# Optimization experiments

Hardware: AMD Instinct MI355X
Metric: run time of the kernel (lower is better)

Reference implementation:

```python
import jax, jax.numpy as jnp
import numpy as np

OUT_H, OUT_W = 128, 128


def _meshgrid(h, w):
    # normalized grid in [-1, 1], homogeneous coords: [3, h*w]
    x_t = jnp.tile(jnp.linspace(-1.0, 1.0, w)[None, :], (h, 1))
    y_t = jnp.tile(jnp.linspace(-1.0, 1.0, h)[:, None], (1, w))
    ones = jnp.ones((h * w,), dtype=jnp.float32)
    return jnp.stack([x_t.ravel(), y_t.ravel(), ones], axis=0)


def _bilinear_sample(im, x, y):
    # im: [B, H, W, C]; x, y: [B, N] pixel-space coords (transformer.py convention)
    B, H, W, C = im.shape
    # map from [-1,1] to pixel coords: x = (x + 1) * W / 2 (original transformer.py)
    x = (x + 1.0) * (W / 2.0)
    y = (y + 1.0) * (H / 2.0)

    x0 = jnp.floor(x).astype(jnp.int32)
    x1 = x0 + 1
    y0 = jnp.floor(y).astype(jnp.int32)
    y1 = y0 + 1

    x0 = jnp.clip(x0, 0, W - 1)
    x1 = jnp.clip(x1, 0, W - 1)
    y0 = jnp.clip(y0, 0, H - 1)
    y1 = jnp.clip(y1, 0, H - 1)

    bidx = jnp.arange(B, dtype=jnp.int32)[:, None]  # [B, 1] broadcasts over N
    Ia = im[bidx, y0, x0]  # [B, N, C]
    Ib = im[bidx, y1, x0]
    Ic = im[bidx, y0, x1]
    Id = im[bidx, y1, x1]

    x0f = x0.astype(jnp.float32)
    x1f = x1.astype(jnp.float32)
    y0f = y0.astype(jnp.float32)
    y1f = y1.astype(jnp.float32)

    wa = ((x1f - x) * (y1f - y))[..., None]
    wb = ((x1f - x) * (y - y0f))[..., None]
    wc = ((x - x0f) * (y1f - y))[..., None]
    wd = ((x - x0f) * (y - y0f))[..., None]

    return wa * Ia + wb * Ib + wc * Ic + wd * Id  # [B, N, C]


def setup_inputs() -> dict:
    key = jax.random.key(0)
    k1, k2 = jax.random.split(key)
    B = 2048
    image = jax.random.uniform(k1, (B, 128, 128, 3), dtype=jnp.float32)
    # near-identity homographies so sampling grids stay numerically sane
    H = jnp.eye(3, dtype=jnp.float32)[None] + 0.1 * jax.random.normal(
        k2, (B, 3, 3), dtype=jnp.float32)
    return {"image": image, "H": H}


def reference(image, H):
    # SpatialTransformer.call: take channel 0, projective warp, bilinear sample
    im = image[:, :, :, 0:1]  # [B, 128, 128, 1]
    B = im.shape[0]
    grid = _meshgrid(OUT_H, OUT_W)  # [3, N]
    T = jnp.einsum('bij,jn->bin', H, grid)  # [B, 3, N]
    z = T[:, 2]
    xs = T[:, 0] / z
    ys = T[:, 1] / z
    out = _bilinear_sample(im, xs, ys)  # [B, N, 1]
    return out.reshape(-1, OUT_H, OUT_W, 1)
```

## Files before the change

kernel.cpp:

```cpp
#include <hip/hip_runtime.h>


#define IMG_H 128
#define IMG_W 128

typedef float f32x2 __attribute__((ext_vector_type(2)));

__global__ __launch_bounds__(256) void st_warp_kernel(
    const float* __restrict__ img,
    const float* __restrict__ Hm,
    float* __restrict__ out)
{
    const int b  = blockIdx.x >> 5;
    const int n0 = ((blockIdx.x & 31) << 9) | (threadIdx.x << 1);
    const int i  = n0 >> 7;
    const int j0 = n0 & 127;

    const float* Hb = Hm + b * 9;
    const float h00 = Hb[0], h01 = Hb[1], h02 = Hb[2];
    const float h10 = Hb[3], h11 = Hb[4], h12 = Hb[5];
    const float h20 = Hb[6], h21 = Hb[7], h22 = Hb[8];

    const float step = 2.0f / 127.0f;
    const float yt = -1.0f + step * (float)i;
    const float* imb = img + (size_t)b * (IMG_H * IMG_W * 3);

    const float xtA = -1.0f + step * (float)j0;
    const float TxA = h00 * xtA + h01 * yt + h02;
    const float TyA = h10 * xtA + h11 * yt + h12;
    const float TzA = h20 * xtA + h21 * yt + h22;
    const float xA = (TxA / TzA + 1.0f) * 64.0f;
    const float yA = (TyA / TzA + 1.0f) * 64.0f;

    const float xtB = -1.0f + step * (float)(j0 + 1);
    const float TxB = h00 * xtB + h01 * yt + h02;
    const float TyB = h10 * xtB + h11 * yt + h12;
    const float TzB = h20 * xtB + h21 * yt + h22;
    const float xB = (TxB / TzB + 1.0f) * 64.0f;
    const float yB = (TyB / TzB + 1.0f) * 64.0f;

    int x0A = (int)fmaxf(fminf(floorf(xA), 2.0e9f), -2.0e9f);
    int y0A = (int)fmaxf(fminf(floorf(yA), 2.0e9f), -2.0e9f);
    int x1A = x0A + 1, y1A = y0A + 1;
    x0A = min(max(x0A, 0), IMG_W - 1); x1A = min(max(x1A, 0), IMG_W - 1);
    y0A = min(max(y0A, 0), IMG_H - 1); y1A = min(max(y1A, 0), IMG_H - 1);

    int x0B = (int)fmaxf(fminf(floorf(xB), 2.0e9f), -2.0e9f);
    int y0B = (int)fmaxf(fminf(floorf(yB), 2.0e9f), -2.0e9f);
    int x1B = x0B + 1, y1B = y0B + 1;
    x0B = min(max(x0B, 0), IMG_W - 1); x1B = min(max(x1B, 0), IMG_W - 1);
    y0B = min(max(y0B, 0), IMG_H - 1); y1B = min(max(y1B, 0), IMG_H - 1);

    const float IaA = imb[(y0A * IMG_W + x0A) * 3];
    const float IbA = imb[(y1A * IMG_W + x0A) * 3];
    const float IcA = imb[(y0A * IMG_W + x1A) * 3];
    const float IdA = imb[(y1A * IMG_W + x1A) * 3];
    const float IaB = imb[(y0B * IMG_W + x0B) * 3];
    const float IbB = imb[(y1B * IMG_W + x0B) * 3];
    const float IcB = imb[(y0B * IMG_W + x1B) * 3];
    const float IdB = imb[(y1B * IMG_W + x1B) * 3];

    f32x2 res;
    {
        const float x0f = (float)x0A, x1f = (float)x1A;
        const float y0f = (float)y0A, y1f = (float)y1A;
        const float wa = (x1f - xA) * (y1f - yA);
        const float wb = (x1f - xA) * (yA - y0f);
        const float wc = (xA - x0f) * (y1f - yA);
        const float wd = (xA - x0f) * (yA - y0f);
        res.x = wa * IaA + wb * IbA + wc * IcA + wd * IdA;
    }
    {
        const float x0f = (float)x0B, x1f = (float)x1B;
        const float y0f = (float)y0B, y1f = (float)y1B;
        const float wa = (x1f - xB) * (y1f - yB);
        const float wb = (x1f - xB) * (yB - y0f);
        const float wc = (xB - x0f) * (y1f - yB);
        const float wd = (xB - x0f) * (yB - y0f);
        res.y = wa * IaB + wb * IbB + wc * IcB + wd * IdB;
    }

    __builtin_nontemporal_store(res,
        reinterpret_cast<f32x2*>(out + (size_t)b * (IMG_H * IMG_W) + n0));
}

extern "C" void kernel_launch(void* const* d_in, const int* in_sizes, int n_in,
                              void* d_out, int out_size, void* d_ws, size_t ws_size,
                              hipStream_t stream) {
    const float* img = (const float*)d_in[0];
    const float* Hm  = (const float*)d_in[1];
    float* out = (float*)d_out;

    const int B = in_sizes[1] / 9;
    const int blocks = B * 32;
    st_warp_kernel<<<blocks, 256, 0, stream>>>(img, Hm, out);
}
```

Before: 126.0 us.

## Fetch bilinear neighbor pairs with vector loads and interleave batches across blocks

Each sample's two horizontally adjacent pixels (channel 0 at stride 3) are now fetched with one unaligned 4-float load per row instead of two scalar loads, halving the gather instruction count. The right-edge column is handled by clamping the load start and selecting the x or w lane. Block indices are also remapped so eight consecutive blocks cover different images at the same row chunk, which changes how work is spread across XCDs and caches. This assumes B is a multiple of 8 and that unaligned 16-byte loads are efficient. It also fetches some unused bytes per load.

```diff
diff --git a/kernel.cpp b/kernel.cpp
--- a/kernel.cpp
+++ b/kernel.cpp
@@ -5,14 +5,21 @@
 #define IMG_W 128
 
 typedef float f32x2 __attribute__((ext_vector_type(2)));
+typedef float f32x4 __attribute__((ext_vector_type(4)));
+typedef f32x4 f32x4_u __attribute__((aligned(4)));
 
 __global__ __launch_bounds__(256) void st_warp_kernel(
     const float* __restrict__ img,
     const float* __restrict__ Hm,
     float* __restrict__ out)
 {
-    const int b  = blockIdx.x >> 5;
-    const int n0 = ((blockIdx.x & 31) << 9) | (threadIdx.x << 1);
+    const int s = blockIdx.x;
+    const int x = s & 7;
+    const int r = s >> 3;
+    const int j = r & 31;
+    const int b = ((r >> 5) << 3) | x;
+
+    const int n0 = (j << 9) | (threadIdx.x << 1);
     const int i  = n0 >> 7;
     const int j0 = n0 & 127;
 
@@ -44,40 +51,46 @@
     int x1A = x0A + 1, y1A = y0A + 1;
     x0A = min(max(x0A, 0), IMG_W - 1); x1A = min(max(x1A, 0), IMG_W - 1);
     y0A = min(max(y0A, 0), IMG_H - 1); y1A = min(max(y1A, 0), IMG_H - 1);
+    const int xlA = min(x0A, IMG_W - 2);
 
     int x0B = (int)fmaxf(fminf(floorf(xB), 2.0e9f), -2.0e9f);
     int y0B = (int)fmaxf(fminf(floorf(yB), 2.0e9f), -2.0e9f);
     int x1B = x0B + 1, y1B = y0B + 1;
     x0B = min(max(x0B, 0), IMG_W - 1); x1B = min(max(x1B, 0), IMG_W - 1);
     y0B = min(max(y0B, 0), IMG_H - 1); y1B = min(max(y1B, 0), IMG_H - 1);
+    const int xlB = min(x0B, IMG_W - 2);
 
-    const float IaA = imb[(y0A * IMG_W + x0A) * 3];
-    const float IbA = imb[(y1A * IMG_W + x0A) * 3];
-    const float IcA = imb[(y0A * IMG_W + x1A) * 3];
-    const float IdA = imb[(y1A * IMG_W + x1A) * 3];
-    const float IaB = imb[(y0B * IMG_W + x0B) * 3];
-    const float IbB = imb[(y1B * IMG_W + x0B) * 3];
-    const float IcB = imb[(y0B * IMG_W + x1B) * 3];
-    const float IdB = imb[(y1B * IMG_W + x1B) * 3];
+    const f32x4 rA0 = *reinterpret_cast<const f32x4_u*>(imb + (y0A * IMG_W + xlA) * 3);
+    const f32x4 rA1 = *reinterpret_cast<const f32x4_u*>(imb + (y1A * IMG_W + xlA) * 3);
+    const f32x4 rB0 = *reinterpret_cast<const f32x4_u*>(imb + (y0B * IMG_W + xlB) * 3);
+    const f32x4 rB1 = *reinterpret_cast<const f32x4_u*>(imb + (y1B * IMG_W + xlB) * 3);
 
     f32x2 res;
     {
+        const float Ia = (x0A > xlA) ? rA0.w : rA0.x;
+        const float Ic = (x1A > xlA) ? rA0.w : rA0.x;
+        const float Ib = (x0A > xlA) ? rA1.w : rA1.x;
+        const float Id = (x1A > xlA) ? rA1.w : rA1.x;
         const float x0f = (float)x0A, x1f = (float)x1A;
         const float y0f = (float)y0A, y1f = (float)y1A;
         const float wa = (x1f - xA) * (y1f - yA);
         const float wb = (x1f - xA) * (yA - y0f);
         const float wc = (xA - x0f) * (y1f - yA);
         const float wd = (xA - x0f) * (yA - y0f);
-        res.x = wa * IaA + wb * IbA + wc * IcA + wd * IdA;
+        res.x = wa * Ia + wb * Ib + wc * Ic + wd * Id;
     }
     {
+        const float Ia = (x0B > xlB) ? rB0.w : rB0.x;
+        const float Ic = (x1B > xlB) ? rB0.w : rB0.x;
+        const float Ib = (x0B > xlB) ? rB1.w : rB1.x;
+        const float Id = (x1B > xlB) ? rB1.w : rB1.x;
         const float x0f = (float)x0B, x1f = (float)x1B;
         const float y0f = (float)y0B, y1f = (float)y1B;
         const float wa = (x1f - xB) * (y1f - yB);
         const float wb = (x1f - xB) * (yB - y0f);
         const float wc = (xB - x0f) * (y1f - yB);
         const float wd = (xB - x0f) * (yB - y0f);
-        res.y = wa * IaB + wb * IbB + wc * IcB + wd * IdB;
+        res.y = wa * Ia + wb * Ib + wc * Ic + wd * Id;
     }
 
     __builtin_nontemporal_store(res,
```

Result: faster. 114.0 us (-9.5%).
